# Kernel tuning notes

Measured on AMD Instinct MI355X. Metric: run time of the kernel, lower is better.

## Reference

```python
import jax, jax.numpy as jnp
import numpy as np

# w_mul = gain * 5**-0.5 * lrmul with gain=sqrt(2), use_wscale=True, lrmul=1
W_MUL = float(2 ** 0.5 * 5 ** -0.5)


def _apply_1q(M, g, q):
    """Apply 2x2 gate g on qubit q (MSB-first) to the rows of matrix M (dim, dim)."""
    dim = M.shape[0]
    Mr = M.reshape(2 ** q, 2, -1)  # (pre, 2, post*dim)
    return jnp.einsum('ab,xby->xay', g, Mr).reshape(dim, dim)


def _fused_xyz_gates(th, n):
    """Per-qubit fused gate Rz(tz) @ Ry(ty) @ Rx(tx); th = [tx_0..n, ty_0..n, tz_0..n]."""
    hx, hy, hz = th[:n] / 2, th[n:2 * n] / 2, th[2 * n:] / 2
    cx, sx = jnp.cos(hx), jnp.sin(hx)
    cy, sy = jnp.cos(hy), jnp.sin(hy)
    z = jnp.zeros_like(hz)
    gx = jnp.stack([jnp.stack([cx + 0j, -1j * sx], -1),
                    jnp.stack([-1j * sx, cx + 0j], -1)], -2)
    gy = jnp.stack([jnp.stack([cy + 0j, -sy + 0j], -1),
                    jnp.stack([sy + 0j, cy + 0j], -1)], -2)
    ez = jnp.exp(-1j * hz)
    gz = jnp.stack([jnp.stack([ez, z + 0j], -1),
                    jnp.stack([z + 0j, jnp.conj(ez)], -1)], -2)
    return jnp.einsum('nab,nbc,ncd->nad', gz, gy, gx).astype(jnp.complex64)


def _cnot_perm(n, c, t):
    """Row permutation implementing CNOT(control=c, target=t), MSB-first bit order."""
    r = np.arange(2 ** n)
    return r ^ (((r >> (n - 1 - c)) & 1) << (n - 1 - t))


def _build_U(weight):
    n = weight.shape[0] // 15
    dim = 2 ** n
    w = weight * W_MUL
    ring_perms = [jnp.asarray(_cnot_perm(n, c, (c + 1) % n)) for c in range(n)]
    U = jnp.eye(dim, dtype=jnp.complex64)
    for layer in range(5):  # 5 XYZ layers, rings of CNOT between them
        g = _fused_xyz_gates(w[3 * n * layer:3 * n * (layer + 1)], n)
        for q in range(n):
            U = _apply_1q(U, g[q], q)
        if layer < 4:
            for p in ring_perms:
                U = U[p]  # CNOT is a row permutation
    return U


def setup_inputs() -> dict:
    key = jax.random.key(0)
    k1, k2 = jax.random.split(key)
    n_qubits = 11
    dim = 2 ** n_qubits
    x = jax.random.normal(k1, (dim, dim), dtype=jnp.float32)
    weight = jax.random.uniform(k2, (15 * n_qubits,), dtype=jnp.float32,
                                minval=0.0, maxval=2.0 * np.pi)
    return {"x": x, "weight": weight}


def reference(x, weight):
    U = _build_U(weight)
    xc = x.astype(jnp.complex64)
    return U @ xc @ U.conj().T
```

## Files before the change

### kernel.cpp

```cpp
#include <hip/hip_runtime.h>

typedef unsigned short u16;
typedef __attribute__((ext_vector_type(8))) short bf16x8;
typedef __attribute__((ext_vector_type(4))) float f32x4;
typedef __attribute__((ext_vector_type(4))) unsigned int u32x4;

#define DIM 2048

__device__ inline u16 f2bf(float f) {
    unsigned u = __builtin_bit_cast(unsigned, f);
    u = (u + 0x7FFFu + ((u >> 16) & 1u)) >> 16;
    return (u16)u;
}

__device__ inline void gl_lds16(const void* g, void* l) {
    __builtin_amdgcn_global_load_lds(
        (const __attribute__((address_space(1))) unsigned int*)g,
        (__attribute__((address_space(3))) unsigned int*)l, 16, 0, 0);
}

struct c32 { float x, y; };
__device__ inline c32 cmul(c32 a, c32 b) { return {a.x*b.x - a.y*b.y, a.x*b.y + a.y*b.x}; }

__device__ inline int slotf(int i) { return i + (i >> 5); }

__global__ __launch_bounds__(256) void build_ut(const float* __restrict__ w,
                                                u16* __restrict__ ut_re,
                                                u16* __restrict__ ut_im) {
    __shared__ alignas(16) float gre[55][4], gim[55][4];
    __shared__ alignas(16) float G4r[5][5][16], G4i[5][5][16];
    __shared__ alignas(16) u16 ptab[DIM];
    __shared__ alignas(16) float vr[DIM + (DIM >> 5)], vi[DIM + (DIM >> 5)];
    const int tid = threadIdx.x;
    const int col = blockIdx.x;

    if (tid < 55) {
        const int layer = tid / 11, q = tid - layer * 11;
        const float WM = 0.63245553203367586f;
        float hx = 0.5f * WM * w[33*layer + q];
        float hy = 0.5f * WM * w[33*layer + 11 + q];
        float hz = 0.5f * WM * w[33*layer + 22 + q];
        float cx = cosf(hx), sx = sinf(hx);
        float cy = cosf(hy), sy = sinf(hy);
        float cz = cosf(hz), sz = sinf(hz);
        c32 m00{cy*cx,  sy*sx}, m01{-sy*cx, -cy*sx};
        c32 m10{sy*cx, -cy*sx}, m11{ cy*cx, -sy*sx};
        c32 em{cz, -sz}, ep{cz, sz};
        c32 r0 = cmul(em, m00), r1 = cmul(em, m01);
        c32 r2 = cmul(ep, m10), r3 = cmul(ep, m11);
        gre[tid][0] = r0.x; gim[tid][0] = r0.y;
        gre[tid][1] = r1.x; gim[tid][1] = r1.y;
        gre[tid][2] = r2.x; gim[tid][2] = r2.y;
        gre[tid][3] = r3.x; gim[tid][3] = r3.y;
    }
    for (int i = tid; i < DIM; i += 256) {
        vr[slotf(i)] = (i == col) ? 1.0f : 0.0f;
        vi[slotf(i)] = 0.0f;
        int jj = i;
        #pragma unroll
        for (int c = 10; c >= 0; --c) {
            int sc = 10 - c;
            int st = 10 - ((c + 1) % 11);
            jj ^= ((jj >> sc) & 1) << st;
        }
        ptab[i] = (u16)slotf(jj);
    }
    __syncthreads();

    for (int t = tid; t < 400; t += 256) {
        int layer = t / 80, r = t % 80, pair = r / 16, e = r % 16;
        int v = e >> 2, vp = e & 3;
        int a = v >> 1, b = v & 1, ap = vp >> 1, bp = vp & 1;
        int gia = layer * 11 + pair;
        int gib = layer * 11 + 6 + pair;
        c32 ga{gre[gia][a*2+ap], gim[gia][a*2+ap]};
        c32 gb{gre[gib][b*2+bp], gim[gib][b*2+bp]};
        c32 pr = cmul(ga, gb);
        G4r[layer][pair][e] = pr.x; G4i[layer][pair][e] = pr.y;
    }
    __syncthreads();

    for (int layer = 0; layer < 5; ++layer) {
        for (int p = 0; p < 5; ++p) {
            const int lo = 4 - p, hi = 10 - p;
            float g4r[16], g4i[16];
            #pragma unroll
            for (int e = 0; e < 16; ++e) {
                g4r[e] = G4r[layer][p][e];
                g4i[e] = G4i[layer][p][e];
            }
            const bool permRead = (layer > 0) && (p == 0);
            if (permRead) {
                float xr[2][4], xi[2][4];
                int es[2][4];
                #pragma unroll
                for (int h = 0; h < 2; ++h) {
                    int g = tid + h * 256;
                    int tmp = ((g >> lo) << (lo + 1)) | (g & ((1 << lo) - 1));
                    int i0  = ((tmp >> hi) << (hi + 1)) | (tmp & ((1 << hi) - 1));
                    #pragma unroll
                    for (int v = 0; v < 4; ++v) {
                        int e = i0 | ((v >> 1) << hi) | ((v & 1) << lo);
                        es[h][v] = slotf(e);
                        int ss = (int)ptab[e];
                        xr[h][v] = vr[ss]; xi[h][v] = vi[ss];
                    }
                }
                __syncthreads();
                #pragma unroll
                for (int h = 0; h < 2; ++h)
                    #pragma unroll
                    for (int v = 0; v < 4; ++v) {
                        float sr = 0.f, si = 0.f;
                        #pragma unroll
                        for (int u = 0; u < 4; ++u) {
                            sr += g4r[v*4+u] * xr[h][u] - g4i[v*4+u] * xi[h][u];
                            si += g4r[v*4+u] * xi[h][u] + g4i[v*4+u] * xr[h][u];
                        }
                        vr[es[h][v]] = sr; vi[es[h][v]] = si;
                    }
                __syncthreads();
            } else {
                #pragma unroll
                for (int h = 0; h < 2; ++h) {
                    int g = tid + h * 256;
                    int tmp = ((g >> lo) << (lo + 1)) | (g & ((1 << lo) - 1));
                    int i0  = ((tmp >> hi) << (hi + 1)) | (tmp & ((1 << hi) - 1));
                    float xr[4], xi[4];
                    int es[4];
                    #pragma unroll
                    for (int v = 0; v < 4; ++v) {
                        int e = i0 | ((v >> 1) << hi) | ((v & 1) << lo);
                        es[v] = slotf(e);
                        xr[v] = vr[es[v]]; xi[v] = vi[es[v]];
                    }
                    #pragma unroll
                    for (int v = 0; v < 4; ++v) {
                        float sr = 0.f, si = 0.f;
                        #pragma unroll
                        for (int u = 0; u < 4; ++u) {
                            sr += g4r[v*4+u] * xr[u] - g4i[v*4+u] * xi[u];
                            si += g4r[v*4+u] * xi[u] + g4i[v*4+u] * xr[u];
                        }
                        vr[es[v]] = sr; vi[es[v]] = si;
                    }
                }
                __syncthreads();
            }
        }
        {
            const int gi = layer * 11 + 5;
            const float g00r = gre[gi][0], g00i = gim[gi][0];
            const float g01r = gre[gi][1], g01i = gim[gi][1];
            const float g10r = gre[gi][2], g10i = gim[gi][2];
            const float g11r = gre[gi][3], g11i = gim[gi][3];
            #pragma unroll
            for (int t = 0; t < 4; ++t) {
                int p2 = tid + t * 256;
                int i0 = ((p2 >> 5) << 6) | (p2 & 31);
                int s0 = slotf(i0), s1 = slotf(i0 + 32);
                float ar = vr[s0], ai = vi[s0];
                float br = vr[s1], bi = vi[s1];
                vr[s0] = g00r*ar - g00i*ai + g01r*br - g01i*bi;
                vi[s0] = g00r*ai + g00i*ar + g01r*bi + g01i*br;
                vr[s1] = g10r*ar - g10i*ai + g11r*br - g11i*bi;
                vi[s1] = g10r*ai + g10i*ar + g11r*bi + g11i*br;
            }
            __syncthreads();
        }
    }
    for (int i = tid; i < DIM; i += 256) {
        ut_re[(size_t)col*DIM + i] = f2bf(vr[slotf(i)]);
        ut_im[(size_t)col*DIM + i] = f2bf(vi[slotf(i)]);
    }
}

__global__ __launch_bounds__(256) void transpose2(const u16* __restrict__ sre,
                                                  const u16* __restrict__ sim,
                                                  u16* __restrict__ dre,
                                                  u16* __restrict__ dim_) {
    const u16* s = blockIdx.z ? sim : sre;
    u16*       d = blockIdx.z ? dim_ : dre;
    __shared__ alignas(16) u16 tile[64][66];
    const int bx = blockIdx.x * 64, by = blockIdx.y * 64;
    for (int e = threadIdx.x; e < 1024; e += 256) {
        int r = e >> 4, c4 = (e & 15) * 4;
        uint2 v = *(const uint2*)(s + (size_t)(by + r) * DIM + bx + c4);
        u16* tp = &tile[r][c4];
        tp[0] = (u16)(v.x); tp[1] = (u16)(v.x >> 16);
        tp[2] = (u16)(v.y); tp[3] = (u16)(v.y >> 16);
    }
    __syncthreads();
    for (int e = threadIdx.x; e < 1024; e += 256) {
        int r = e >> 4, c4 = (e & 15) * 4;
        unsigned lo = (unsigned)tile[c4][r]     | ((unsigned)tile[c4+1][r] << 16);
        unsigned hi = (unsigned)tile[c4+2][r]   | ((unsigned)tile[c4+3][r] << 16);
        *(uint2*)(d + (size_t)(bx + r) * DIM + by + c4) = make_uint2(lo, hi);
    }
}

__global__ __launch_bounds__(256, 2) void gemm_stage1(
        const u16* __restrict__ ure, const u16* __restrict__ uim,
        const float* __restrict__ x,
        u16* __restrict__ pt, u16* __restrict__ qt) {
    __shared__ alignas(16) u16 Ab[2][2][128*32], Bx[2][2][128*32];
    const u16* A  = blockIdx.z ? uim : ure;
    u16*      dst = blockIdx.z ? qt  : pt;
    const int tid  = threadIdx.x;
    const int lane = tid & 63, w = tid >> 6;
    const int m0 = blockIdx.y * 128, n0 = blockIdx.x * 128;
    const int wm = (w >> 1) * 64, wn = (w & 1) * 64;
    const int ml = lane & 15, quad = lane >> 4;

    f32x4 acc[4][4];
    #pragma unroll
    for (int i = 0; i < 4; ++i)
        #pragma unroll
        for (int j = 0; j < 4; ++j) {
            f32x4 z = {0.f, 0.f, 0.f, 0.f};
            acc[i][j] = z;
        }

    auto stage = [&](int b, int k0) {
        #pragma unroll
        for (int pn = 0; pn < 2; ++pn) {
            #pragma unroll
            for (int t = 0; t < 2; ++t) {
                int ci = t * 256 + tid;
                int r = ci >> 2, c = ci & 3;
                size_t goA = ((size_t)(m0 + r) * DIM + k0 + pn * 32) * 2 + c * 16;
                gl_lds16((const char*)A + goA, (char*)Ab[b][pn] + ci * 16);
                const float4* src = (const float4*)(x + (size_t)(n0 + r) * DIM + k0 + pn * 32 + c * 8);
                float4 v0 = src[0], v1 = src[1];
                u32x4 pk;
                pk.x = (unsigned)f2bf(v0.x) | ((unsigned)f2bf(v0.y) << 16);
                pk.y = (unsigned)f2bf(v0.z) | ((unsigned)f2bf(v0.w) << 16);
                pk.z = (unsigned)f2bf(v1.x) | ((unsigned)f2bf(v1.y) << 16);
                pk.w = (unsigned)f2bf(v1.z) | ((unsigned)f2bf(v1.w) << 16);
                *(u32x4*)((char*)Bx[b][pn] + ci * 16) = pk;
            }
        }
    };

    stage(0, 0);
    __syncthreads();

    for (int k0 = 0; k0 < DIM; k0 += 64) {
        const int cb = (k0 >> 6) & 1;
        if (k0 + 64 < DIM) stage(cb ^ 1, k0 + 64);

        #pragma unroll
        for (int pn = 0; pn < 2; ++pn) {
            bf16x8 af[4], bf[4];
            #pragma unroll
            for (int i = 0; i < 4; ++i) {
                af[i] = *(const bf16x8*)(Ab[cb][pn] + (wm + i*16 + ml) * 32 + quad * 8);
                bf[i] = *(const bf16x8*)(Bx[cb][pn] + (wn + i*16 + ml) * 32 + quad * 8);
            }
            #pragma unroll
            for (int i = 0; i < 4; ++i)
                #pragma unroll
                for (int j = 0; j < 4; ++j)
                    acc[i][j] = __builtin_amdgcn_mfma_f32_16x16x32_bf16(af[i], bf[j], acc[i][j], 0, 0, 0);
        }
        __syncthreads();
    }
    #pragma unroll
    for (int i = 0; i < 4; ++i)
        #pragma unroll
        for (int j = 0; j < 4; ++j) {
            int row = m0 + wm + i*16 + quad*4;
            int col = n0 + wn + j*16 + ml;
            #pragma unroll
            for (int r = 0; r < 4; ++r)
                dst[(size_t)(row + r) * DIM + col] = f2bf(acc[i][j][r]);
        }
}

__global__ __launch_bounds__(256, 2) void gemm_stage2_atomic(
        const u16* __restrict__ ure, const u16* __restrict__ uim,
        const u16* __restrict__ pt, const u16* __restrict__ qt,
        float* __restrict__ out) {
    __shared__ alignas(16) u16 Ab[2][2][128*32], Bb[2][2][128*32];
    const u16* A = blockIdx.z ? uim : ure;
    const u16* B = blockIdx.z ? qt  : pt;
    const int tid  = threadIdx.x;
    const int lane = tid & 63, w = tid >> 6;
    const int m0 = blockIdx.y * 128, n0 = blockIdx.x * 128;
    const int wm = (w >> 1) * 64, wn = (w & 1) * 64;
    const int ml = lane & 15, quad = lane >> 4;

    f32x4 acc[4][4];
    #pragma unroll
    for (int i = 0; i < 4; ++i)
        #pragma unroll
        for (int j = 0; j < 4; ++j) {
            f32x4 z = {0.f, 0.f, 0.f, 0.f};
            acc[i][j] = z;
        }

    auto stage = [&](int b, int k0) {
        #pragma unroll
        for (int pn = 0; pn < 2; ++pn) {
            #pragma unroll
            for (int t = 0; t < 2; ++t) {
                int ci = t * 256 + tid;
                int r = ci >> 2, c = ci & 3;
                size_t goA = ((size_t)(m0 + r) * DIM + k0 + pn * 32) * 2 + c * 16;
                size_t goB = ((size_t)(n0 + r) * DIM + k0 + pn * 32) * 2 + c * 16;
                gl_lds16((const char*)A + goA, (char*)Ab[b][pn] + ci * 16);
                gl_lds16((const char*)B + goB, (char*)Bb[b][pn] + ci * 16);
            }
        }
    };

    stage(0, 0);
    __syncthreads();

    for (int k0 = 0; k0 < DIM; k0 += 64) {
        const int cb = (k0 >> 6) & 1;
        if (k0 + 64 < DIM) stage(cb ^ 1, k0 + 64);

        #pragma unroll
        for (int pn = 0; pn < 2; ++pn) {
            bf16x8 af[4], bf[4];
            #pragma unroll
            for (int i = 0; i < 4; ++i) {
                af[i] = *(const bf16x8*)(Ab[cb][pn] + (wm + i*16 + ml) * 32 + quad * 8);
                bf[i] = *(const bf16x8*)(Bb[cb][pn] + (wn + i*16 + ml) * 32 + quad * 8);
            }
            #pragma unroll
            for (int i = 0; i < 4; ++i)
                #pragma unroll
                for (int j = 0; j < 4; ++j)
                    acc[i][j] = __builtin_amdgcn_mfma_f32_16x16x32_bf16(af[i], bf[j], acc[i][j], 0, 0, 0);
        }
        __syncthreads();
    }
    #pragma unroll
    for (int i = 0; i < 4; ++i)
        #pragma unroll
        for (int j = 0; j < 4; ++j) {
            int row = m0 + wm + i*16 + quad*4;
            int col = n0 + wn + j*16 + ml;
            #pragma unroll
            for (int r = 0; r < 4; ++r)
                unsafeAtomicAdd(&out[(size_t)(row + r) * DIM + col], acc[i][j][r]);
        }
}

__global__ __launch_bounds__(256, 1) void gemm_stage2_cplx(
        const u16* __restrict__ ure, const u16* __restrict__ uim,
        const u16* __restrict__ pt, const u16* __restrict__ qt,
        float2* __restrict__ out, size_t out_lim) {
    __shared__ alignas(16) u16 Ar[128*32], Ai[128*32], Bp[128*32], Bq[128*32];
    const int tid  = threadIdx.x;
    const int lane = tid & 63, w = tid >> 6;
    const int m0 = blockIdx.y * 128, n0 = blockIdx.x * 128;
    const int wm = (w >> 1) * 64, wn = (w & 1) * 64;
    const int ml = lane & 15, quad = lane >> 4;

    f32x4 accR[4][4], accI[4][4];
    #pragma unroll
    for (int i = 0; i < 4; ++i)
        #pragma unroll
        for (int j = 0; j < 4; ++j) {
            f32x4 z = {0.f, 0.f, 0.f, 0.f};
            accR[i][j] = z; accI[i][j] = z;
        }

    for (int k0 = 0; k0 < DIM; k0 += 32) {
        #pragma unroll
        for (int t = 0; t < 2; ++t) {
            int ci = t * 256 + tid;
            int r = ci >> 2, c = ci & 3;
            size_t goA = ((size_t)(m0 + r) * DIM + k0) * 2 + c * 16;
            size_t goB = ((size_t)(n0 + r) * DIM + k0) * 2 + c * 16;
            gl_lds16((const char*)ure + goA, (char*)Ar + ci * 16);
            gl_lds16((const char*)uim + goA, (char*)Ai + ci * 16);
            gl_lds16((const char*)pt  + goB, (char*)Bp + ci * 16);
            gl_lds16((const char*)qt  + goB, (char*)Bq + ci * 16);
        }
        __syncthreads();
        bf16x8 ar[4], ai[4], bp[4], bq[4];
        #pragma unroll
        for (int i = 0; i < 4; ++i) {
            ar[i] = *(const bf16x8*)(Ar + (wm + i*16 + ml) * 32 + quad * 8);
            ai[i] = *(const bf16x8*)(Ai + (wm + i*16 + ml) * 32 + quad * 8);
            bp[i] = *(const bf16x8*)(Bp + (wn + i*16 + ml) * 32 + quad * 8);
            bq[i] = *(const bf16x8*)(Bq + (wn + i*16 + ml) * 32 + quad * 8);
        }
        #pragma unroll
        for (int i = 0; i < 4; ++i)
            #pragma unroll
            for (int j = 0; j < 4; ++j) {
                accR[i][j] = __builtin_amdgcn_mfma_f32_16x16x32_bf16(ar[i], bp[j], accR[i][j], 0, 0, 0);
                accR[i][j] = __builtin_amdgcn_mfma_f32_16x16x32_bf16(ai[i], bq[j], accR[i][j], 0, 0, 0);
                accI[i][j] = __builtin_amdgcn_mfma_f32_16x16x32_bf16(ai[i], bp[j], accI[i][j], 0, 0, 0);
                f32x4 t2 = __builtin_amdgcn_mfma_f32_16x16x32_bf16(ar[i], bq[j], {0.f,0.f,0.f,0.f}, 0, 0, 0);
                accI[i][j] -= t2;
            }
        __syncthreads();
    }
    #pragma unroll
    for (int i = 0; i < 4; ++i)
        #pragma unroll
        for (int j = 0; j < 4; ++j) {
            int row = m0 + wm + i*16 + quad*4;
            int col = n0 + wn + j*16 + ml;
            #pragma unroll
            for (int r = 0; r < 4; ++r) {
                size_t idx = (size_t)(row + r) * DIM + col;
                if (idx < out_lim)
                    out[idx] = make_float2(accR[i][j][r], accI[i][j][r]);
            }
        }
}

extern "C" void kernel_launch(void* const* d_in, const int* in_sizes, int n_in,
                              void* d_out, int out_size, void* d_ws, size_t ws_size,
                              hipStream_t stream) {
    int xi = (in_sizes[0] >= in_sizes[1]) ? 0 : 1;
    const float* x = (const float*)d_in[xi];
    const float* w = (const float*)d_in[1 - xi];

    char* ws = (char*)d_ws;
    const size_t P = (size_t)DIM * DIM * 2;
    if (ws_size < 4 * P) return;

    u16* ut_re = (u16*)(ws);
    u16* ut_im = (u16*)(ws + P);
    u16* u_re  = (u16*)(ws + 2*P);
    u16* u_im  = (u16*)(ws + 3*P);
    u16* pt    = ut_re;
    u16* qt    = ut_im;

    build_ut<<<DIM, 256, 0, stream>>>(w, ut_re, ut_im);
    transpose2<<<dim3(32, 32, 2), 256, 0, stream>>>(ut_re, ut_im, u_re, u_im);
    gemm_stage1<<<dim3(16, 16, 2), 256, 0, stream>>>(u_re, u_im, x, pt, qt);

    if (out_size == DIM * DIM) {
        hipMemsetAsync(d_out, 0, (size_t)DIM * DIM * sizeof(float), stream);
        gemm_stage2_atomic<<<dim3(16, 16, 2), 256, 0, stream>>>(u_re, u_im, pt, qt,
                                                                (float*)d_out);
    } else {
        gemm_stage2_cplx<<<dim3(16, 16), 256, 0, stream>>>(u_re, u_im, pt, qt,
                                                           (float2*)d_out,
                                                           (size_t)out_size / 2);
    }
}
```

Measured before the change: 269.0 us.

## Apply gates as sequential radix-8 butterflies with interleaved complex LDS layout

Replaces the per-pair fused 4x4 Kronecker gate products with sequential 2x2 butterflies over three qubits per pass (radix-8), plus a final two-qubit pass. This cuts passes per layer from six to four, which means fewer barriers and LDS round-trips, and it lowers the FLOPs per element. It also stores the state as interleaved float2 with a new padding scheme, and drops the G4 precompute stage. The build_ut kernel is only part of the pipeline, so the overall effect depends on its share of the total time.

```diff
diff --git a/kernel.cpp b/kernel.cpp
--- a/kernel.cpp
+++ b/kernel.cpp
@@ -22,15 +22,24 @@
 struct c32 { float x, y; };
 __device__ inline c32 cmul(c32 a, c32 b) { return {a.x*b.x - a.y*b.y, a.x*b.y + a.y*b.x}; }
 
-__device__ inline int slotf(int i) { return i + (i >> 5); }
+__device__ inline int slot2(int i) { return i + (i >> 4); }
+
+__device__ inline void bfly(float2 g0, float2 g1, float2 g2, float2 g3,
+                            float2& u, float2& w) {
+    float2 nu, nw;
+    nu.x = g0.x*u.x - g0.y*u.y + g1.x*w.x - g1.y*w.y;
+    nu.y = g0.x*u.y + g0.y*u.x + g1.x*w.y + g1.y*w.x;
+    nw.x = g2.x*u.x - g2.y*u.y + g3.x*w.x - g3.y*w.y;
+    nw.y = g2.x*u.y + g2.y*u.x + g3.x*w.y + g3.y*w.x;
+    u = nu; w = nw;
+}
 
 __global__ __launch_bounds__(256) void build_ut(const float* __restrict__ w,
                                                 u16* __restrict__ ut_re,
                                                 u16* __restrict__ ut_im) {
-    __shared__ alignas(16) float gre[55][4], gim[55][4];
-    __shared__ alignas(16) float G4r[5][5][16], G4i[5][5][16];
+    __shared__ alignas(16) float2 gg[55][4];
     __shared__ alignas(16) u16 ptab[DIM];
-    __shared__ alignas(16) float vr[DIM + (DIM >> 5)], vi[DIM + (DIM >> 5)];
+    __shared__ alignas(16) float2 V[DIM + (DIM >> 4)];
     const int tid = threadIdx.x;
     const int col = blockIdx.x;
 
@@ -48,14 +57,13 @@
         c32 em{cz, -sz}, ep{cz, sz};
         c32 r0 = cmul(em, m00), r1 = cmul(em, m01);
         c32 r2 = cmul(ep, m10), r3 = cmul(ep, m11);
-        gre[tid][0] = r0.x; gim[tid][0] = r0.y;
-        gre[tid][1] = r1.x; gim[tid][1] = r1.y;
-        gre[tid][2] = r2.x; gim[tid][2] = r2.y;
-        gre[tid][3] = r3.x; gim[tid][3] = r3.y;
+        gg[tid][0] = make_float2(r0.x, r0.y);
+        gg[tid][1] = make_float2(r1.x, r1.y);
+        gg[tid][2] = make_float2(r2.x, r2.y);
+        gg[tid][3] = make_float2(r3.x, r3.y);
     }
     for (int i = tid; i < DIM; i += 256) {
-        vr[slotf(i)] = (i == col) ? 1.0f : 0.0f;
-        vi[slotf(i)] = 0.0f;
+        V[slot2(i)] = make_float2((i == col) ? 1.0f : 0.0f, 0.0f);
         int jj = i;
         #pragma unroll
         for (int c = 10; c >= 0; --c) {
@@ -63,115 +71,66 @@
             int st = 10 - ((c + 1) % 11);
             jj ^= ((jj >> sc) & 1) << st;
         }
-        ptab[i] = (u16)slotf(jj);
+        ptab[i] = (u16)slot2(jj);
     }
     __syncthreads();
 
-    for (int t = tid; t < 400; t += 256) {
-        int layer = t / 80, r = t % 80, pair = r / 16, e = r % 16;
-        int v = e >> 2, vp = e & 3;
-        int a = v >> 1, b = v & 1, ap = vp >> 1, bp = vp & 1;
-        int gia = layer * 11 + pair;
-        int gib = layer * 11 + 6 + pair;
-        c32 ga{gre[gia][a*2+ap], gim[gia][a*2+ap]};
-        c32 gb{gre[gib][b*2+bp], gim[gib][b*2+bp]};
-        c32 pr = cmul(ga, gb);
-        G4r[layer][pair][e] = pr.x; G4i[layer][pair][e] = pr.y;
-    }
-    __syncthreads();
+    auto round3 = [&](int b2, int b1, int b0, int gq2, int gq1, int gq0,
+                      bool permRead) {
+        int x = tid;
+        x = ((x >> b0) << (b0 + 1)) | (x & ((1 << b0) - 1));
+        x = ((x >> b1) << (b1 + 1)) | (x & ((1 << b1) - 1));
+        x = ((x >> b2) << (b2 + 1)) | (x & ((1 << b2) - 1));
+        float2 v[8]; int sl[8];
+        #pragma unroll
+        for (int j = 0; j < 8; ++j) {
+            int e = x | ((j >> 2) << b2) | (((j >> 1) & 1) << b1) | ((j & 1) << b0);
+            sl[j] = slot2(e);
+            v[j] = V[permRead ? (int)ptab[e] : sl[j]];
+        }
+        if (permRead) __syncthreads();
+        {   float2 g0 = gg[gq2][0], g1 = gg[gq2][1], g2 = gg[gq2][2], g3 = gg[gq2][3];
+            bfly(g0,g1,g2,g3, v[0], v[4]); bfly(g0,g1,g2,g3, v[1], v[5]);
+            bfly(g0,g1,g2,g3, v[2], v[6]); bfly(g0,g1,g2,g3, v[3], v[7]); }
+        {   float2 g0 = gg[gq1][0], g1 = gg[gq1][1], g2 = gg[gq1][2], g3 = gg[gq1][3];
+            bfly(g0,g1,g2,g3, v[0], v[2]); bfly(g0,g1,g2,g3, v[1], v[3]);
+            bfly(g0,g1,g2,g3, v[4], v[6]); bfly(g0,g1,g2,g3, v[5], v[7]); }
+        {   float2 g0 = gg[gq0][0], g1 = gg[gq0][1], g2 = gg[gq0][2], g3 = gg[gq0][3];
+            bfly(g0,g1,g2,g3, v[0], v[1]); bfly(g0,g1,g2,g3, v[2], v[3]);
+            bfly(g0,g1,g2,g3, v[4], v[5]); bfly(g0,g1,g2,g3, v[6], v[7]); }
+        #pragma unroll
+        for (int j = 0; j < 8; ++j) V[sl[j]] = v[j];
+        __syncthreads();
+    };
+
+    auto round2 = [&](int gq1, int gq0) {
+        float2 g10 = gg[gq1][0], g11 = gg[gq1][1], g12 = gg[gq1][2], g13 = gg[gq1][3];
+        float2 g00 = gg[gq0][0], g01 = gg[gq0][1], g02 = gg[gq0][2], g03 = gg[gq0][3];
+        #pragma unroll
+        for (int h = 0; h < 2; ++h) {
+            int i0 = (tid + h * 256) << 2;
+            float2 v[4]; int sl[4];
+            #pragma unroll
+            for (int j = 0; j < 4; ++j) { sl[j] = slot2(i0 | j); v[j] = V[sl[j]]; }
+            bfly(g10,g11,g12,g13, v[0], v[2]); bfly(g10,g11,g12,g13, v[1], v[3]);
+            bfly(g00,g01,g02,g03, v[0], v[1]); bfly(g00,g01,g02,g03, v[2], v[3]);
+            #pragma unroll
+            for (int j = 0; j < 4; ++j) V[sl[j]] = v[j];
+        }
+        __syncthreads();
+    };
 
     for (int layer = 0; layer < 5; ++layer) {
-        for (int p = 0; p < 5; ++p) {
-            const int lo = 4 - p, hi = 10 - p;
-            float g4r[16], g4i[16];
-            #pragma unroll
-            for (int e = 0; e < 16; ++e) {
-                g4r[e] = G4r[layer][p][e];
-                g4i[e] = G4i[layer][p][e];
-            }
-            const bool permRead = (layer > 0) && (p == 0);
-            if (permRead) {
-                float xr[2][4], xi[2][4];
-                int es[2][4];
-                #pragma unroll
-                for (int h = 0; h < 2; ++h) {
-                    int g = tid + h * 256;
-                    int tmp = ((g >> lo) << (lo + 1)) | (g & ((1 << lo) - 1));
-                    int i0  = ((tmp >> hi) << (hi + 1)) | (tmp & ((1 << hi) - 1));
-                    #pragma unroll
-                    for (int v = 0; v < 4; ++v) {
-                        int e = i0 | ((v >> 1) << hi) | ((v & 1) << lo);
-                        es[h][v] = slotf(e);
-                        int ss = (int)ptab[e];
-                        xr[h][v] = vr[ss]; xi[h][v] = vi[ss];
-                    }
-                }
-                __syncthreads();
-                #pragma unroll
-                for (int h = 0; h < 2; ++h)
-                    #pragma unroll
-                    for (int v = 0; v < 4; ++v) {
-                        float sr = 0.f, si = 0.f;
-                        #pragma unroll
-                        for (int u = 0; u < 4; ++u) {
-                            sr += g4r[v*4+u] * xr[h][u] - g4i[v*4+u] * xi[h][u];
-                            si += g4r[v*4+u] * xi[h][u] + g4i[v*4+u] * xr[h][u];
-                        }
-                        vr[es[h][v]] = sr; vi[es[h][v]] = si;
-                    }
-                __syncthreads();
-            } else {
-                #pragma unroll
-                for (int h = 0; h < 2; ++h) {
-                    int g = tid + h * 256;
-                    int tmp = ((g >> lo) << (lo + 1)) | (g & ((1 << lo) - 1));
-                    int i0  = ((tmp >> hi) << (hi + 1)) | (tmp & ((1 << hi) - 1));
-                    float xr[4], xi[4];
-                    int es[4];
-                    #pragma unroll
-                    for (int v = 0; v < 4; ++v) {
-                        int e = i0 | ((v >> 1) << hi) | ((v & 1) << lo);
-                        es[v] = slotf(e);
-                        xr[v] = vr[es[v]]; xi[v] = vi[es[v]];
-                    }
-                    #pragma unroll
-                    for (int v = 0; v < 4; ++v) {
-                        float sr = 0.f, si = 0.f;
-                        #pragma unroll
-                        for (int u = 0; u < 4; ++u) {
-                            sr += g4r[v*4+u] * xr[u] - g4i[v*4+u] * xi[u];
-                            si += g4r[v*4+u] * xi[u] + g4i[v*4+u] * xr[u];
-                        }
-                        vr[es[v]] = sr; vi[es[v]] = si;
-                    }
-                }
-                __syncthreads();
-            }
-        }
-        {
-            const int gi = layer * 11 + 5;
-            const float g00r = gre[gi][0], g00i = gim[gi][0];
-            const float g01r = gre[gi][1], g01i = gim[gi][1];
-            const float g10r = gre[gi][2], g10i = gim[gi][2];
-            const float g11r = gre[gi][3], g11i = gim[gi][3];
-            #pragma unroll
-            for (int t = 0; t < 4; ++t) {
-                int p2 = tid + t * 256;
-                int i0 = ((p2 >> 5) << 6) | (p2 & 31);
-                int s0 = slotf(i0), s1 = slotf(i0 + 32);
-                float ar = vr[s0], ai = vi[s0];
-                float br = vr[s1], bi = vi[s1];
-                vr[s0] = g00r*ar - g00i*ai + g01r*br - g01i*bi;
-                vi[s0] = g00r*ai + g00i*ar + g01r*bi + g01i*br;
-                vr[s1] = g10r*ar - g10i*ai + g11r*br - g11i*bi;
-                vi[s1] = g10r*ai + g10i*ar + g11r*bi + g11i*br;
-            }
-            __syncthreads();
-        }
+        const int gb = layer * 11;
+        round3(10, 9, 8, gb + 0, gb + 1, gb + 2, layer > 0);
+        round3( 7, 6, 5, gb + 3, gb + 4, gb + 5, false);
+        round3( 4, 3, 2, gb + 6, gb + 7, gb + 8, false);
+        round2(gb + 9, gb + 10);
     }
     for (int i = tid; i < DIM; i += 256) {
-        ut_re[(size_t)col*DIM + i] = f2bf(vr[slotf(i)]);
-        ut_im[(size_t)col*DIM + i] = f2bf(vi[slotf(i)]);
+        float2 v = V[slot2(i)];
+        ut_re[(size_t)col*DIM + i] = f2bf(v.x);
+        ut_im[(size_t)col*DIM + i] = f2bf(v.y);
     }
 }
 
```

New measurement: 264.9 us. About the same (-1.5%).
